# Kernel optimization log

Hardware: AMD Instinct MI355X
Metric: run time of the kernel (lower is better)

The kernel has to match this reference:

```python
import jax, jax.numpy as jnp
import numpy as np

N = 100000      # nodes
E = 1_600_000   # edges (avg degree 16)
IN, HID, OUT = 64, 64, 32


def setup_inputs() -> dict:
    key = jax.random.key(0)
    k1, k2, k3, k4, k5, k6 = jax.random.split(key, 6)
    x = jax.random.uniform(k1, (N, IN), dtype=jnp.float32)
    edge_index = jax.random.randint(k2, (2, E), 0, N, dtype=jnp.int32)
    # GCNConv weights (glorot-ish scale) and biases
    W1 = jax.random.normal(k3, (IN, HID), dtype=jnp.float32) * (1.0 / np.sqrt(IN))
    b1 = jnp.zeros((HID,), dtype=jnp.float32)
    W2 = jax.random.normal(k4, (HID, OUT), dtype=jnp.float32) * (1.0 / np.sqrt(HID))
    b2 = jnp.zeros((OUT,), dtype=jnp.float32)
    return {"x": x, "edge_index": edge_index, "W1": W1, "b1": b1, "W2": W2, "b2": b2}


def reference(x, edge_index, W1, b1, W2, b2):
    n = x.shape[0]
    # PyG GCNConv: add self-loops, symmetric deg^{-1/2} normalization
    loops = jnp.arange(n, dtype=edge_index.dtype)
    src = jnp.concatenate([edge_index[0], loops])  # message sources
    dst = jnp.concatenate([edge_index[1], loops])  # message targets
    ones = jnp.ones(src.shape[0], dtype=x.dtype)
    deg = jax.ops.segment_sum(ones, dst, num_segments=n)
    dinv = jnp.where(deg > 0, jax.lax.rsqrt(deg), 0.0)
    norm = dinv[src] * dinv[dst]  # [E+N]

    def gcn_conv(h, W, b):
        h = h @ W                          # [n, d_out]
        msg = h[src] * norm[:, None]       # gather + edge-normalize
        agg = jax.ops.segment_sum(msg, dst, num_segments=n)  # scatter-add
        return agg + b

    h = jax.nn.relu(gcn_conv(x, W1, b1))
    return gcn_conv(h, W2, b2)
```

## Files before the change

kernel.cpp:

```cpp
#include <hip/hip_runtime.h>
#include <hip/hip_fp16.h>


#define BSHIFT 8
#define BNODES 256
#define NB 256
#define CAP 5120

union H8 {
    uint4 u;
    __half2 h[4];
};

__device__ inline float2 u2f2(unsigned u) {
    union { unsigned x; __half2 h; } c;
    c.x = u;
    return __half22float2(c.h);
}
__device__ inline unsigned f2u(float a, float b) {
    union { unsigned x; __half2 h; } c;
    c.h = __floats2half2_rn(a, b);
    return c.x;
}

__global__ __launch_bounds__(256) void scatter_kernel(
    const int* __restrict__ src, const int* __restrict__ dst,
    int* __restrict__ cur, int* __restrict__ buf, int E) {
    __shared__ int h[512];
    __shared__ int curl[512];
    int t = threadIdx.x, b = blockIdx.x;
    for (int i = t; i < 512; i += 256) h[i] = 0;
    __syncthreads();
    int per = (E + NB - 1) / NB;
    int lo = b * per;
    int hi = min(lo + per, E);
    for (int i = lo + t; i < hi; i += 256) atomicAdd(&h[dst[i] >> BSHIFT], 1);
    __syncthreads();
    for (int i = t; i < 512; i += 256) {
        int c = h[i];
        curl[i] = c ? atomicAdd(&cur[i], c) : 0;
    }
    __syncthreads();
    for (int i = lo + t; i < hi; i += 256) {
        int d = dst[i];
        int bin = d >> BSHIFT;
        int loc = atomicAdd(&curl[bin], 1);
        if (loc < CAP)
            buf[(size_t)bin * CAP + loc] = (src[i] << BSHIFT) | (d & (BNODES - 1));
    }
}

__global__ __launch_bounds__(256) void bsort_kernel(
    const int* __restrict__ cur, int* __restrict__ buf,
    int2* __restrict__ off2, float* __restrict__ dinv, int N) {
    __shared__ int stage[CAP];
    __shared__ int h[BNODES];
    __shared__ int c2[BNODES];
    int t = threadIdx.x, b = blockIdx.x;
    int cnt = min(cur[b], CAP);
    int base = b * CAP;
    for (int i = t; i < cnt; i += 256) stage[i] = buf[base + i];
    h[t] = 0;
    __syncthreads();
    for (int i = t; i < cnt; i += 256)
        atomicAdd(&h[stage[i] & (BNODES - 1)], 1);
    __syncthreads();
    int deg = h[t];
#pragma unroll
    for (int d = 1; d < BNODES; d <<= 1) {
        int v = (t >= d) ? h[t - d] : 0;
        __syncthreads();
        h[t] += v;
        __syncthreads();
    }
    int excl = h[t] - deg;
    c2[t] = excl;
    int node = (b << BSHIFT) + t;
    if (node < N) {
        off2[node] = make_int2(base + excl, base + excl + deg);
        dinv[node] = rsqrtf((float)(deg + 1));
    }
    __syncthreads();
    for (int i = t; i < cnt; i += 256) {
        int p = stage[i];
        int pos = atomicAdd(&c2[p & (BNODES - 1)], 1);
        buf[base + pos] = p >> BSHIFT;
    }
}

__global__ __launch_bounds__(256) void gemm1_kernel(
    const float* __restrict__ x, const float* __restrict__ W1,
    const float* __restrict__ dinv, __half* __restrict__ hsh, int N) {
    __shared__ float4 Ws[64 * 16];
    int t = threadIdx.x;
    const float4* W4 = (const float4*)W1;
    for (int i = t; i < 1024; i += 256) Ws[i] = W4[i];
    __syncthreads();
    int c = t & 3;
    int rg = t >> 2;
    int r0 = blockIdx.x * 256 + rg * 4;
    if (r0 >= N) return;
    int nm1 = N - 1;
    float4 acc[4][4];
#pragma unroll
    for (int r = 0; r < 4; r++)
#pragma unroll
        for (int j = 0; j < 4; j++) acc[r][j] = make_float4(0.f, 0.f, 0.f, 0.f);
    const float4* x4 = (const float4*)x;
    for (int k4 = 0; k4 < 16; k4++) {
        float4 xv[4];
#pragma unroll
        for (int r = 0; r < 4; r++)
            xv[r] = x4[(size_t)min(r0 + r, nm1) * 16 + k4];
#pragma unroll
        for (int kk = 0; kk < 4; kk++) {
            const float4* wr = &Ws[(k4 * 4 + kk) * 16 + c * 4];
            float4 w0 = wr[0], w1 = wr[1], w2 = wr[2], w3 = wr[3];
#pragma unroll
            for (int r = 0; r < 4; r++) {
                float a = (kk == 0) ? xv[r].x : (kk == 1) ? xv[r].y
                          : (kk == 2) ? xv[r].z : xv[r].w;
                acc[r][0].x += a * w0.x; acc[r][0].y += a * w0.y;
                acc[r][0].z += a * w0.z; acc[r][0].w += a * w0.w;
                acc[r][1].x += a * w1.x; acc[r][1].y += a * w1.y;
                acc[r][1].z += a * w1.z; acc[r][1].w += a * w1.w;
                acc[r][2].x += a * w2.x; acc[r][2].y += a * w2.y;
                acc[r][2].z += a * w2.z; acc[r][2].w += a * w2.w;
                acc[r][3].x += a * w3.x; acc[r][3].y += a * w3.y;
                acc[r][3].z += a * w3.z; acc[r][3].w += a * w3.w;
            }
        }
    }
#pragma unroll
    for (int r = 0; r < 4; r++) {
        int row = r0 + r;
        if (row >= N) break;
        float di = dinv[row];
        uint4* ha = (uint4*)(hsh + (size_t)row * 64);
        H8 p0, p1;
        p0.h[0] = __floats2half2_rn(acc[r][0].x * di, acc[r][0].y * di);
        p0.h[1] = __floats2half2_rn(acc[r][0].z * di, acc[r][0].w * di);
        p0.h[2] = __floats2half2_rn(acc[r][1].x * di, acc[r][1].y * di);
        p0.h[3] = __floats2half2_rn(acc[r][1].z * di, acc[r][1].w * di);
        p1.h[0] = __floats2half2_rn(acc[r][2].x * di, acc[r][2].y * di);
        p1.h[1] = __floats2half2_rn(acc[r][2].z * di, acc[r][2].w * di);
        p1.h[2] = __floats2half2_rn(acc[r][3].x * di, acc[r][3].y * di);
        p1.h[3] = __floats2half2_rn(acc[r][3].z * di, acc[r][3].w * di);
        ha[c * 2 + 0] = p0.u;
        ha[c * 2 + 1] = p1.u;
    }
}

__global__ __launch_bounds__(256) void agg1gemm2_kernel(
    const uint4* __restrict__ hsh4, const int* __restrict__ ssrc,
    const int2* __restrict__ off2, const float* __restrict__ dinv,
    const float* __restrict__ b1, const float* __restrict__ W2,
    __half* __restrict__ gsh, int N) {
    __shared__ float4 Ws2[64 * 8];
    int t = threadIdx.x;
    const float4* W24 = (const float4*)W2;
    for (int i = t; i < 512; i += 256) Ws2[i] = W24[i];
    __syncthreads();
    int lane = t & 63;
    int wid = (blockIdx.x * 256 + t) >> 6;
    int node = wid * 8 + (lane >> 3);
    int fi = lane & 7;
    if (node >= N) return;
    int2 lh = off2[node];
    int lo = lh.x, hi = lh.y;
    float di = dinv[node];
    H8 sv;
    sv.u = hsh4[(size_t)node * 8 + fi];
    float2 a0 = __half22float2(sv.h[0]);
    float2 a1 = __half22float2(sv.h[1]);
    float2 a2 = __half22float2(sv.h[2]);
    float2 a3 = __half22float2(sv.h[3]);
    float2 c0 = make_float2(0.f, 0.f), c1 = make_float2(0.f, 0.f);
    float2 c2 = make_float2(0.f, 0.f), c3 = make_float2(0.f, 0.f);
    int hm1 = hi - 1;
    for (int e = lo; e < hi; e += 8) {
        int i1 = min(e + 1, hm1), i2 = min(e + 2, hm1), i3 = min(e + 3, hm1);
        int i4 = min(e + 4, hm1), i5 = min(e + 5, hm1), i6 = min(e + 6, hm1),
            i7 = min(e + 7, hm1);
        int s0 = __builtin_nontemporal_load(&ssrc[e]);
        int s1 = __builtin_nontemporal_load(&ssrc[i1]);
        int s2 = __builtin_nontemporal_load(&ssrc[i2]);
        int s3 = __builtin_nontemporal_load(&ssrc[i3]);
        int s4 = __builtin_nontemporal_load(&ssrc[i4]);
        int s5 = __builtin_nontemporal_load(&ssrc[i5]);
        int s6 = __builtin_nontemporal_load(&ssrc[i6]);
        int s7 = __builtin_nontemporal_load(&ssrc[i7]);
        H8 v0, v1, v2, v3, v4, v5, v6, v7;
        v0.u = hsh4[(size_t)s0 * 8 + fi];
        v1.u = hsh4[(size_t)s1 * 8 + fi];
        v2.u = hsh4[(size_t)s2 * 8 + fi];
        v3.u = hsh4[(size_t)s3 * 8 + fi];
        v4.u = hsh4[(size_t)s4 * 8 + fi];
        v5.u = hsh4[(size_t)s5 * 8 + fi];
        v6.u = hsh4[(size_t)s6 * 8 + fi];
        v7.u = hsh4[(size_t)s7 * 8 + fi];
        float m1 = (e + 1 < hi) ? 1.f : 0.f;
        float m2 = (e + 2 < hi) ? 1.f : 0.f;
        float m3 = (e + 3 < hi) ? 1.f : 0.f;
        float m4 = (e + 4 < hi) ? 1.f : 0.f;
        float m5 = (e + 5 < hi) ? 1.f : 0.f;
        float m6 = (e + 6 < hi) ? 1.f : 0.f;
        float m7 = (e + 7 < hi) ? 1.f : 0.f;
#pragma unroll
        for (int q = 0; q < 4; q++) {
            float2* aA = (q == 0) ? &a0 : (q == 1) ? &a1 : (q == 2) ? &a2 : &a3;
            float2* cA = (q == 0) ? &c0 : (q == 1) ? &c1 : (q == 2) ? &c2 : &c3;
            float2 f0 = __half22float2(v0.h[q]);
            float2 f1 = __half22float2(v1.h[q]);
            float2 f2 = __half22float2(v2.h[q]);
            float2 f3 = __half22float2(v3.h[q]);
            float2 f4 = __half22float2(v4.h[q]);
            float2 f5 = __half22float2(v5.h[q]);
            float2 f6 = __half22float2(v6.h[q]);
            float2 f7 = __half22float2(v7.h[q]);
            aA->x += f0.x + m1 * f1.x + m2 * f2.x + m3 * f3.x;
            aA->y += f0.y + m1 * f1.y + m2 * f2.y + m3 * f3.y;
            cA->x += m4 * f4.x + m5 * f5.x + m6 * f6.x + m7 * f7.x;
            cA->y += m4 * f4.y + m5 * f5.y + m6 * f6.y + m7 * f7.y;
        }
    }
    float4 bl = ((const float4*)b1)[fi * 2];
    float4 bh = ((const float4*)b1)[fi * 2 + 1];
    float r0 = fmaxf((a0.x + c0.x) * di + bl.x, 0.f);
    float r1 = fmaxf((a0.y + c0.y) * di + bl.y, 0.f);
    float r2 = fmaxf((a1.x + c1.x) * di + bl.z, 0.f);
    float r3 = fmaxf((a1.y + c1.y) * di + bl.w, 0.f);
    float r4 = fmaxf((a2.x + c2.x) * di + bh.x, 0.f);
    float r5 = fmaxf((a2.y + c2.y) * di + bh.y, 0.f);
    float r6 = fmaxf((a3.x + c3.x) * di + bh.z, 0.f);
    float r7 = fmaxf((a3.y + c3.y) * di + bh.w, 0.f);
    unsigned pk0 = f2u(r0, r1), pk1 = f2u(r2, r3);
    unsigned pk2 = f2u(r4, r5), pk3 = f2u(r6, r7);
    float4 acc2 = make_float4(0.f, 0.f, 0.f, 0.f);
#pragma unroll
    for (int s = 0; s < 8; s++) {
        int sl = (fi + s) & 7;
        unsigned u0 = __shfl(pk0, sl, 8);
        unsigned u1 = __shfl(pk1, sl, 8);
        unsigned u2 = __shfl(pk2, sl, 8);
        unsigned u3 = __shfl(pk3, sl, 8);
        float2 f0 = u2f2(u0), f1 = u2f2(u1), f2 = u2f2(u2), f3 = u2f2(u3);
        const float4* wr = &Ws2[sl * 64 + fi];
        float4 w;
        w = wr[0];
        acc2.x += f0.x * w.x; acc2.y += f0.x * w.y;
        acc2.z += f0.x * w.z; acc2.w += f0.x * w.w;
        w = wr[8];
        acc2.x += f0.y * w.x; acc2.y += f0.y * w.y;
        acc2.z += f0.y * w.z; acc2.w += f0.y * w.w;
        w = wr[16];
        acc2.x += f1.x * w.x; acc2.y += f1.x * w.y;
        acc2.z += f1.x * w.z; acc2.w += f1.x * w.w;
        w = wr[24];
        acc2.x += f1.y * w.x; acc2.y += f1.y * w.y;
        acc2.z += f1.y * w.z; acc2.w += f1.y * w.w;
        w = wr[32];
        acc2.x += f2.x * w.x; acc2.y += f2.x * w.y;
        acc2.z += f2.x * w.z; acc2.w += f2.x * w.w;
        w = wr[40];
        acc2.x += f2.y * w.x; acc2.y += f2.y * w.y;
        acc2.z += f2.y * w.z; acc2.w += f2.y * w.w;
        w = wr[48];
        acc2.x += f3.x * w.x; acc2.y += f3.x * w.y;
        acc2.z += f3.x * w.z; acc2.w += f3.x * w.w;
        w = wr[56];
        acc2.x += f3.y * w.x; acc2.y += f3.y * w.y;
        acc2.z += f3.y * w.z; acc2.w += f3.y * w.w;
    }
    uint2 pg;
    pg.x = f2u(acc2.x * di, acc2.y * di);
    pg.y = f2u(acc2.z * di, acc2.w * di);
    ((uint2*)gsh)[(size_t)node * 8 + fi] = pg;
}

__global__ __launch_bounds__(256) void agg2_kernel(
    const uint4* __restrict__ gsh4, const int* __restrict__ ssrc,
    const int2* __restrict__ off2, const float* __restrict__ dinv,
    const float* __restrict__ b2, float4* __restrict__ out4, int N) {
    int lane = threadIdx.x & 63;
    int wid = (blockIdx.x * 256 + threadIdx.x) >> 6;
    int node = wid * 16 + (lane >> 2);
    int fi = lane & 3;
    if (node >= N) return;
    int2 lh = off2[node];
    int lo = lh.x, hi = lh.y;
    float di = dinv[node];
    H8 sv;
    sv.u = gsh4[(size_t)node * 4 + fi];
    float2 a0 = __half22float2(sv.h[0]);
    float2 a1 = __half22float2(sv.h[1]);
    float2 a2 = __half22float2(sv.h[2]);
    float2 a3 = __half22float2(sv.h[3]);
    float2 c0 = make_float2(0.f, 0.f), c1 = make_float2(0.f, 0.f);
    float2 c2 = make_float2(0.f, 0.f), c3 = make_float2(0.f, 0.f);
    int hm1 = hi - 1;
    for (int e = lo; e < hi; e += 8) {
        int i1 = min(e + 1, hm1), i2 = min(e + 2, hm1), i3 = min(e + 3, hm1);
        int i4 = min(e + 4, hm1), i5 = min(e + 5, hm1), i6 = min(e + 6, hm1),
            i7 = min(e + 7, hm1);
        int s0 = __builtin_nontemporal_load(&ssrc[e]);
        int s1 = __builtin_nontemporal_load(&ssrc[i1]);
        int s2 = __builtin_nontemporal_load(&ssrc[i2]);
        int s3 = __builtin_nontemporal_load(&ssrc[i3]);
        int s4 = __builtin_nontemporal_load(&ssrc[i4]);
        int s5 = __builtin_nontemporal_load(&ssrc[i5]);
        int s6 = __builtin_nontemporal_load(&ssrc[i6]);
        int s7 = __builtin_nontemporal_load(&ssrc[i7]);
        H8 v0, v1, v2, v3, v4, v5, v6, v7;
        v0.u = gsh4[(size_t)s0 * 4 + fi];
        v1.u = gsh4[(size_t)s1 * 4 + fi];
        v2.u = gsh4[(size_t)s2 * 4 + fi];
        v3.u = gsh4[(size_t)s3 * 4 + fi];
        v4.u = gsh4[(size_t)s4 * 4 + fi];
        v5.u = gsh4[(size_t)s5 * 4 + fi];
        v6.u = gsh4[(size_t)s6 * 4 + fi];
        v7.u = gsh4[(size_t)s7 * 4 + fi];
        float m1 = (e + 1 < hi) ? 1.f : 0.f;
        float m2 = (e + 2 < hi) ? 1.f : 0.f;
        float m3 = (e + 3 < hi) ? 1.f : 0.f;
        float m4 = (e + 4 < hi) ? 1.f : 0.f;
        float m5 = (e + 5 < hi) ? 1.f : 0.f;
        float m6 = (e + 6 < hi) ? 1.f : 0.f;
        float m7 = (e + 7 < hi) ? 1.f : 0.f;
#pragma unroll
        for (int q = 0; q < 4; q++) {
            float2* aA = (q == 0) ? &a0 : (q == 1) ? &a1 : (q == 2) ? &a2 : &a3;
            float2* cA = (q == 0) ? &c0 : (q == 1) ? &c1 : (q == 2) ? &c2 : &c3;
            float2 f0 = __half22float2(v0.h[q]);
            float2 f1 = __half22float2(v1.h[q]);
            float2 f2 = __half22float2(v2.h[q]);
            float2 f3 = __half22float2(v3.h[q]);
            float2 f4 = __half22float2(v4.h[q]);
            float2 f5 = __half22float2(v5.h[q]);
            float2 f6 = __half22float2(v6.h[q]);
            float2 f7 = __half22float2(v7.h[q]);
            aA->x += f0.x + m1 * f1.x + m2 * f2.x + m3 * f3.x;
            aA->y += f0.y + m1 * f1.y + m2 * f2.y + m3 * f3.y;
            cA->x += m4 * f4.x + m5 * f5.x + m6 * f6.x + m7 * f7.x;
            cA->y += m4 * f4.y + m5 * f5.y + m6 * f6.y + m7 * f7.y;
        }
    }
    float4 bl = ((const float4*)b2)[fi * 2];
    float4 bh = ((const float4*)b2)[fi * 2 + 1];
    float4 r0, r1;
    r0.x = (a0.x + c0.x) * di + bl.x;
    r0.y = (a0.y + c0.y) * di + bl.y;
    r0.z = (a1.x + c1.x) * di + bl.z;
    r0.w = (a1.y + c1.y) * di + bl.w;
    r1.x = (a2.x + c2.x) * di + bh.x;
    r1.y = (a2.y + c2.y) * di + bh.y;
    r1.z = (a3.x + c3.x) * di + bh.z;
    r1.w = (a3.y + c3.y) * di + bh.w;
    out4[(size_t)node * 8 + fi * 2 + 0] = r0;
    out4[(size_t)node * 8 + fi * 2 + 1] = r1;
}

extern "C" void kernel_launch(void* const* d_in, const int* in_sizes, int n_in,
                              void* d_out, int out_size, void* d_ws,
                              size_t ws_size, hipStream_t stream) {
    const float* x  = (const float*)d_in[0];
    const int* ei   = (const int*)d_in[1];
    const float* W1 = (const float*)d_in[2];
    const float* b1 = (const float*)d_in[3];
    const float* W2 = (const float*)d_in[4];
    const float* b2 = (const float*)d_in[5];
    int N = in_sizes[0] / 64;
    int E = in_sizes[1] / 2;
    const int* src = ei;
    const int* dst = ei + E;
    int B = (N + BNODES - 1) >> BSHIFT;

    char* ws = (char*)d_ws;
    size_t o = 0;
    auto align16 = [&o]() { o = (o + 15) & ~(size_t)15; };
    int* cur    = (int*)(ws + o); o += 512 * 4; align16();
    int* buf    = (int*)(ws + o); o += (size_t)B * CAP * 4; align16();
    int2* off2  = (int2*)(ws + o); o += (size_t)N * 8; align16();
    float* dinv = (float*)(ws + o); o += (size_t)N * 4; align16();
    __half* hsh = (__half*)(ws + o); o += (size_t)N * 64 * 2; align16();
    __half* gsh = (__half*)(ws + o); o += (size_t)N * 32 * 2; align16();
    float* outp = (float*)d_out;

    hipMemsetAsync(cur, 0, 512 * 4, stream);
    scatter_kernel<<<NB, 256, 0, stream>>>(src, dst, cur, buf, E);
    bsort_kernel<<<B, 256, 0, stream>>>(cur, buf, off2, dinv, N);
    gemm1_kernel<<<(N + 255) / 256, 256, 0, stream>>>(x, W1, dinv, hsh, N);
    agg1gemm2_kernel<<<(N + 31) / 32, 256, 0, stream>>>(
        (const uint4*)hsh, buf, off2, dinv, b1, W2, gsh, N);
    agg2_kernel<<<(N + 63) / 64, 256, 0, stream>>>(
        (const uint4*)gsh, buf, off2, dinv, b2, (float4*)outp, N);
}
```

Before: 207.4 us.

## Bucket nodes by degree class to balance warp work in aggregation kernels

The sort kernel now groups nodes into eight degree classes (in steps of 8 edges) and writes a per-class node order list with global class counts. Both aggregation kernels map thread groups to nodes through this order, so nodes sharing a wavefront have similar edge counts and loop trip counts. The aim is less divergence and idle lanes in the edge loops. In exchange it adds an indirection lookup per node, extra atomics and writes in bsort, and loses the locality of consecutive node IDs for the per-node loads and output stores.

```diff
diff --git a/kernel.cpp b/kernel.cpp
--- a/kernel.cpp
+++ b/kernel.cpp
@@ -21,6 +21,18 @@
     union { unsigned x; __half2 h; } c;
     c.h = __floats2half2_rn(a, b);
     return c.x;
+}
+
+__device__ inline int rank_to_node(int g, const int* __restrict__ clscnt,
+                                   const int* __restrict__ order, int N) {
+    int pre = 0, node = -1;
+#pragma unroll
+    for (int c = 0; c < 8; c++) {
+        int cc = clscnt[c];
+        if (node < 0 && g < pre + cc) node = order[c * N + (g - pre)];
+        pre += cc;
+    }
+    return node;
 }
 
 __global__ __launch_bounds__(256) void scatter_kernel(
@@ -52,20 +64,29 @@
 
 __global__ __launch_bounds__(256) void bsort_kernel(
     const int* __restrict__ cur, int* __restrict__ buf,
-    int2* __restrict__ off2, float* __restrict__ dinv, int N) {
+    int2* __restrict__ off2, float* __restrict__ dinv,
+    int* __restrict__ order, int* __restrict__ clscnt, int N) {
     __shared__ int stage[CAP];
     __shared__ int h[BNODES];
     __shared__ int c2[BNODES];
+    __shared__ int ch[8];
+    __shared__ int cbase[8];
     int t = threadIdx.x, b = blockIdx.x;
     int cnt = min(cur[b], CAP);
     int base = b * CAP;
     for (int i = t; i < cnt; i += 256) stage[i] = buf[base + i];
     h[t] = 0;
+    if (t < 8) ch[t] = 0;
     __syncthreads();
     for (int i = t; i < cnt; i += 256)
         atomicAdd(&h[stage[i] & (BNODES - 1)], 1);
     __syncthreads();
     int deg = h[t];
+    int node = (b << BSHIFT) + t;
+    bool valid = node < N;
+    int cls = min((deg + 7) >> 3, 7);
+    int loc = 0;
+    if (valid) loc = atomicAdd(&ch[cls], 1);
 #pragma unroll
     for (int d = 1; d < BNODES; d <<= 1) {
         int v = (t >= d) ? h[t - d] : 0;
@@ -75,12 +96,13 @@
     }
     int excl = h[t] - deg;
     c2[t] = excl;
-    int node = (b << BSHIFT) + t;
-    if (node < N) {
+    if (t < 8) cbase[t] = ch[t] ? atomicAdd(&clscnt[t], ch[t]) : 0;
+    if (valid) {
         off2[node] = make_int2(base + excl, base + excl + deg);
         dinv[node] = rsqrtf((float)(deg + 1));
     }
     __syncthreads();
+    if (valid) order[cls * N + cbase[cls] + loc] = node;
     for (int i = t; i < cnt; i += 256) {
         int p = stage[i];
         int pos = atomicAdd(&c2[p & (BNODES - 1)], 1);
@@ -154,6 +176,7 @@
 __global__ __launch_bounds__(256) void agg1gemm2_kernel(
     const uint4* __restrict__ hsh4, const int* __restrict__ ssrc,
     const int2* __restrict__ off2, const float* __restrict__ dinv,
+    const int* __restrict__ order, const int* __restrict__ clscnt,
     const float* __restrict__ b1, const float* __restrict__ W2,
     __half* __restrict__ gsh, int N) {
     __shared__ float4 Ws2[64 * 8];
@@ -163,9 +186,10 @@
     __syncthreads();
     int lane = t & 63;
     int wid = (blockIdx.x * 256 + t) >> 6;
-    int node = wid * 8 + (lane >> 3);
+    int g = wid * 8 + (lane >> 3);
     int fi = lane & 7;
-    if (node >= N) return;
+    if (g >= N) return;
+    int node = rank_to_node(g, clscnt, order, N);
     int2 lh = off2[node];
     int lo = lh.x, hi = lh.y;
     float di = dinv[node];
@@ -281,12 +305,14 @@
 __global__ __launch_bounds__(256) void agg2_kernel(
     const uint4* __restrict__ gsh4, const int* __restrict__ ssrc,
     const int2* __restrict__ off2, const float* __restrict__ dinv,
+    const int* __restrict__ order, const int* __restrict__ clscnt,
     const float* __restrict__ b2, float4* __restrict__ out4, int N) {
     int lane = threadIdx.x & 63;
     int wid = (blockIdx.x * 256 + threadIdx.x) >> 6;
-    int node = wid * 16 + (lane >> 2);
+    int g = wid * 16 + (lane >> 2);
     int fi = lane & 3;
-    if (node >= N) return;
+    if (g >= N) return;
+    int node = rank_to_node(g, clscnt, order, N);
     int2 lh = off2[node];
     int lo = lh.x, hi = lh.y;
     float di = dinv[node];
@@ -378,20 +404,24 @@
     char* ws = (char*)d_ws;
     size_t o = 0;
     auto align16 = [&o]() { o = (o + 15) & ~(size_t)15; };
-    int* cur    = (int*)(ws + o); o += 512 * 4; align16();
+    int* cur    = (int*)(ws + o); o += 520 * 4; align16();
+    int* clscnt = cur + 512;
     int* buf    = (int*)(ws + o); o += (size_t)B * CAP * 4; align16();
     int2* off2  = (int2*)(ws + o); o += (size_t)N * 8; align16();
     float* dinv = (float*)(ws + o); o += (size_t)N * 4; align16();
+    int* order  = (int*)(ws + o); o += (size_t)N * 8 * 4; align16();
     __half* hsh = (__half*)(ws + o); o += (size_t)N * 64 * 2; align16();
     __half* gsh = (__half*)(ws + o); o += (size_t)N * 32 * 2; align16();
     float* outp = (float*)d_out;
 
-    hipMemsetAsync(cur, 0, 512 * 4, stream);
+    hipMemsetAsync(cur, 0, 520 * 4, stream);
     scatter_kernel<<<NB, 256, 0, stream>>>(src, dst, cur, buf, E);
-    bsort_kernel<<<B, 256, 0, stream>>>(cur, buf, off2, dinv, N);
+    bsort_kernel<<<B, 256, 0, stream>>>(cur, buf, off2, dinv, order, clscnt,
+                                        N);
     gemm1_kernel<<<(N + 255) / 256, 256, 0, stream>>>(x, W1, dinv, hsh, N);
     agg1gemm2_kernel<<<(N + 31) / 32, 256, 0, stream>>>(
-        (const uint4*)hsh, buf, off2, dinv, b1, W2, gsh, N);
+        (const uint4*)hsh, buf, off2, dinv, order, clscnt, b1, W2, gsh, N);
     agg2_kernel<<<(N + 63) / 64, 256, 0, stream>>>(
-        (const uint4*)gsh, buf, off2, dinv, b2, (float4*)outp, N);
-}
+        (const uint4*)gsh, buf, off2, dinv, order, clscnt, b2, (float4*)outp,
+        N);
+}
```

Result: slower. 239.3 us (+15.4%).

## Compute degrees in scatter via global atomics and co-launch bucket sort with gemm1

Applied to the files above, without the earlier changes.

The scatter kernel now counts per-node in-degree with global atomics, so degrees are known before the bucket sort. That lets the bucket sort and the first GEMM, which no longer depends on sort output, run as disjoint block ranges of a single launch. dinv is recomputed on the fly from deg with rsqrtf instead of being stored. This removes one kernel launch and serialization point. In exchange it adds 1.6M global atomics in scatter and a larger memset.

```diff
diff --git a/kernel.cpp b/kernel.cpp
--- a/kernel.cpp
+++ b/kernel.cpp
@@ -25,7 +25,8 @@
 
 __global__ __launch_bounds__(256) void scatter_kernel(
     const int* __restrict__ src, const int* __restrict__ dst,
-    int* __restrict__ cur, int* __restrict__ buf, int E) {
+    int* __restrict__ cur, int* __restrict__ deg, int* __restrict__ buf,
+    int E) {
     __shared__ int h[512];
     __shared__ int curl[512];
     int t = threadIdx.x, b = blockIdx.x;
@@ -47,113 +48,111 @@
         int loc = atomicAdd(&curl[bin], 1);
         if (loc < CAP)
             buf[(size_t)bin * CAP + loc] = (src[i] << BSHIFT) | (d & (BNODES - 1));
-    }
-}
-
-__global__ __launch_bounds__(256) void bsort_kernel(
+        atomicAdd(&deg[d], 1);
+    }
+}
+
+__global__ __launch_bounds__(256) void sortgemm_kernel(
     const int* __restrict__ cur, int* __restrict__ buf,
-    int2* __restrict__ off2, float* __restrict__ dinv, int N) {
-    __shared__ int stage[CAP];
-    __shared__ int h[BNODES];
-    __shared__ int c2[BNODES];
-    int t = threadIdx.x, b = blockIdx.x;
-    int cnt = min(cur[b], CAP);
-    int base = b * CAP;
-    for (int i = t; i < cnt; i += 256) stage[i] = buf[base + i];
-    h[t] = 0;
-    __syncthreads();
-    for (int i = t; i < cnt; i += 256)
-        atomicAdd(&h[stage[i] & (BNODES - 1)], 1);
-    __syncthreads();
-    int deg = h[t];
-#pragma unroll
-    for (int d = 1; d < BNODES; d <<= 1) {
-        int v = (t >= d) ? h[t - d] : 0;
+    const int* __restrict__ deg, int2* __restrict__ off2,
+    const float* __restrict__ x, const float* __restrict__ W1,
+    __half* __restrict__ hsh, int N, int B) {
+    __shared__ int smem[CAP + 512];
+    int t = threadIdx.x;
+    if ((int)blockIdx.x < B) {
+        int b = blockIdx.x;
+        int* stage = smem;
+        int* c2 = smem + CAP;
+        int* sc = smem + CAP + 256;
+        int cnt = min(cur[b], CAP);
+        int base = b * CAP;
+        for (int i = t; i < cnt; i += 256) stage[i] = buf[base + i];
+        int node = (b << BSHIFT) + t;
+        int dg = (node < N) ? deg[node] : 0;
+        sc[t] = dg;
         __syncthreads();
-        h[t] += v;
+#pragma unroll
+        for (int d = 1; d < BNODES; d <<= 1) {
+            int v = (t >= d) ? sc[t - d] : 0;
+            __syncthreads();
+            sc[t] += v;
+            __syncthreads();
+        }
+        int excl = sc[t] - dg;
+        c2[t] = excl;
+        if (node < N)
+            off2[node] = make_int2(base + excl, base + excl + dg);
         __syncthreads();
-    }
-    int excl = h[t] - deg;
-    c2[t] = excl;
-    int node = (b << BSHIFT) + t;
-    if (node < N) {
-        off2[node] = make_int2(base + excl, base + excl + deg);
-        dinv[node] = rsqrtf((float)(deg + 1));
-    }
-    __syncthreads();
-    for (int i = t; i < cnt; i += 256) {
-        int p = stage[i];
-        int pos = atomicAdd(&c2[p & (BNODES - 1)], 1);
-        buf[base + pos] = p >> BSHIFT;
-    }
-}
-
-__global__ __launch_bounds__(256) void gemm1_kernel(
-    const float* __restrict__ x, const float* __restrict__ W1,
-    const float* __restrict__ dinv, __half* __restrict__ hsh, int N) {
-    __shared__ float4 Ws[64 * 16];
-    int t = threadIdx.x;
-    const float4* W4 = (const float4*)W1;
-    for (int i = t; i < 1024; i += 256) Ws[i] = W4[i];
-    __syncthreads();
-    int c = t & 3;
-    int rg = t >> 2;
-    int r0 = blockIdx.x * 256 + rg * 4;
-    if (r0 >= N) return;
-    int nm1 = N - 1;
-    float4 acc[4][4];
-#pragma unroll
-    for (int r = 0; r < 4; r++)
-#pragma unroll
-        for (int j = 0; j < 4; j++) acc[r][j] = make_float4(0.f, 0.f, 0.f, 0.f);
-    const float4* x4 = (const float4*)x;
-    for (int k4 = 0; k4 < 16; k4++) {
-        float4 xv[4];
+        for (int i = t; i < cnt; i += 256) {
+            int p = stage[i];
+            int pos = atomicAdd(&c2[p & (BNODES - 1)], 1);
+            buf[base + pos] = p >> BSHIFT;
+        }
+    } else {
+        float4* Ws = (float4*)smem;
+        const float4* W4 = (const float4*)W1;
+        for (int i = t; i < 1024; i += 256) Ws[i] = W4[i];
+        __syncthreads();
+        int c = t & 3;
+        int rg = t >> 2;
+        int r0 = ((int)blockIdx.x - B) * 256 + rg * 4;
+        if (r0 >= N) return;
+        int nm1 = N - 1;
+        float4 acc[4][4];
 #pragma unroll
         for (int r = 0; r < 4; r++)
-            xv[r] = x4[(size_t)min(r0 + r, nm1) * 16 + k4];
-#pragma unroll
-        for (int kk = 0; kk < 4; kk++) {
-            const float4* wr = &Ws[(k4 * 4 + kk) * 16 + c * 4];
-            float4 w0 = wr[0], w1 = wr[1], w2 = wr[2], w3 = wr[3];
-#pragma unroll
-            for (int r = 0; r < 4; r++) {
-                float a = (kk == 0) ? xv[r].x : (kk == 1) ? xv[r].y
-                          : (kk == 2) ? xv[r].z : xv[r].w;
-                acc[r][0].x += a * w0.x; acc[r][0].y += a * w0.y;
-                acc[r][0].z += a * w0.z; acc[r][0].w += a * w0.w;
-                acc[r][1].x += a * w1.x; acc[r][1].y += a * w1.y;
-                acc[r][1].z += a * w1.z; acc[r][1].w += a * w1.w;
-                acc[r][2].x += a * w2.x; acc[r][2].y += a * w2.y;
-                acc[r][2].z += a * w2.z; acc[r][2].w += a * w2.w;
-                acc[r][3].x += a * w3.x; acc[r][3].y += a * w3.y;
-                acc[r][3].z += a * w3.z; acc[r][3].w += a * w3.w;
+#pragma unroll
+            for (int j = 0; j < 4; j++)
+                acc[r][j] = make_float4(0.f, 0.f, 0.f, 0.f);
+        const float4* x4 = (const float4*)x;
+        for (int k4 = 0; k4 < 16; k4++) {
+            float4 xv[4];
+#pragma unroll
+            for (int r = 0; r < 4; r++)
+                xv[r] = x4[(size_t)min(r0 + r, nm1) * 16 + k4];
+#pragma unroll
+            for (int kk = 0; kk < 4; kk++) {
+                const float4* wr = &Ws[(k4 * 4 + kk) * 16 + c * 4];
+                float4 w0 = wr[0], w1 = wr[1], w2 = wr[2], w3 = wr[3];
+#pragma unroll
+                for (int r = 0; r < 4; r++) {
+                    float a = (kk == 0) ? xv[r].x : (kk == 1) ? xv[r].y
+                              : (kk == 2) ? xv[r].z : xv[r].w;
+                    acc[r][0].x += a * w0.x; acc[r][0].y += a * w0.y;
+                    acc[r][0].z += a * w0.z; acc[r][0].w += a * w0.w;
+                    acc[r][1].x += a * w1.x; acc[r][1].y += a * w1.y;
+                    acc[r][1].z += a * w1.z; acc[r][1].w += a * w1.w;
+                    acc[r][2].x += a * w2.x; acc[r][2].y += a * w2.y;
+                    acc[r][2].z += a * w2.z; acc[r][2].w += a * w2.w;
+                    acc[r][3].x += a * w3.x; acc[r][3].y += a * w3.y;
+                    acc[r][3].z += a * w3.z; acc[r][3].w += a * w3.w;
+                }
             }
         }
-    }
-#pragma unroll
-    for (int r = 0; r < 4; r++) {
-        int row = r0 + r;
-        if (row >= N) break;
-        float di = dinv[row];
-        uint4* ha = (uint4*)(hsh + (size_t)row * 64);
-        H8 p0, p1;
-        p0.h[0] = __floats2half2_rn(acc[r][0].x * di, acc[r][0].y * di);
-        p0.h[1] = __floats2half2_rn(acc[r][0].z * di, acc[r][0].w * di);
-        p0.h[2] = __floats2half2_rn(acc[r][1].x * di, acc[r][1].y * di);
-        p0.h[3] = __floats2half2_rn(acc[r][1].z * di, acc[r][1].w * di);
-        p1.h[0] = __floats2half2_rn(acc[r][2].x * di, acc[r][2].y * di);
-        p1.h[1] = __floats2half2_rn(acc[r][2].z * di, acc[r][2].w * di);
-        p1.h[2] = __floats2half2_rn(acc[r][3].x * di, acc[r][3].y * di);
-        p1.h[3] = __floats2half2_rn(acc[r][3].z * di, acc[r][3].w * di);
-        ha[c * 2 + 0] = p0.u;
-        ha[c * 2 + 1] = p1.u;
+#pragma unroll
+        for (int r = 0; r < 4; r++) {
+            int row = r0 + r;
+            if (row >= N) break;
+            float di = rsqrtf((float)(deg[row] + 1));
+            uint4* ha = (uint4*)(hsh + (size_t)row * 64);
+            H8 p0, p1;
+            p0.h[0] = __floats2half2_rn(acc[r][0].x * di, acc[r][0].y * di);
+            p0.h[1] = __floats2half2_rn(acc[r][0].z * di, acc[r][0].w * di);
+            p0.h[2] = __floats2half2_rn(acc[r][1].x * di, acc[r][1].y * di);
+            p0.h[3] = __floats2half2_rn(acc[r][1].z * di, acc[r][1].w * di);
+            p1.h[0] = __floats2half2_rn(acc[r][2].x * di, acc[r][2].y * di);
+            p1.h[1] = __floats2half2_rn(acc[r][2].z * di, acc[r][2].w * di);
+            p1.h[2] = __floats2half2_rn(acc[r][3].x * di, acc[r][3].y * di);
+            p1.h[3] = __floats2half2_rn(acc[r][3].z * di, acc[r][3].w * di);
+            ha[c * 2 + 0] = p0.u;
+            ha[c * 2 + 1] = p1.u;
+        }
     }
 }
 
 __global__ __launch_bounds__(256) void agg1gemm2_kernel(
     const uint4* __restrict__ hsh4, const int* __restrict__ ssrc,
-    const int2* __restrict__ off2, const float* __restrict__ dinv,
+    const int2* __restrict__ off2, const int* __restrict__ deg,
     const float* __restrict__ b1, const float* __restrict__ W2,
     __half* __restrict__ gsh, int N) {
     __shared__ float4 Ws2[64 * 8];
@@ -168,7 +167,7 @@
     if (node >= N) return;
     int2 lh = off2[node];
     int lo = lh.x, hi = lh.y;
-    float di = dinv[node];
+    float di = rsqrtf((float)(deg[node] + 1));
     H8 sv;
     sv.u = hsh4[(size_t)node * 8 + fi];
     float2 a0 = __half22float2(sv.h[0]);
@@ -280,7 +279,7 @@
 
 __global__ __launch_bounds__(256) void agg2_kernel(
     const uint4* __restrict__ gsh4, const int* __restrict__ ssrc,
-    const int2* __restrict__ off2, const float* __restrict__ dinv,
+    const int2* __restrict__ off2, const int* __restrict__ deg,
     const float* __restrict__ b2, float4* __restrict__ out4, int N) {
     int lane = threadIdx.x & 63;
     int wid = (blockIdx.x * 256 + threadIdx.x) >> 6;
@@ -289,7 +288,7 @@
     if (node >= N) return;
     int2 lh = off2[node];
     int lo = lh.x, hi = lh.y;
-    float di = dinv[node];
+    float di = rsqrtf((float)(deg[node] + 1));
     H8 sv;
     sv.u = gsh4[(size_t)node * 4 + fi];
     float2 a0 = __half22float2(sv.h[0]);
@@ -374,24 +373,25 @@
     const int* src = ei;
     const int* dst = ei + E;
     int B = (N + BNODES - 1) >> BSHIFT;
+    int G = (N + 255) / 256;
 
     char* ws = (char*)d_ws;
     size_t o = 0;
     auto align16 = [&o]() { o = (o + 15) & ~(size_t)15; };
-    int* cur    = (int*)(ws + o); o += 512 * 4; align16();
+    int* cur    = (int*)(ws + o); o += 512 * 4;
+    int* deg    = (int*)(ws + o); o += (size_t)N * 4; align16();
     int* buf    = (int*)(ws + o); o += (size_t)B * CAP * 4; align16();
     int2* off2  = (int2*)(ws + o); o += (size_t)N * 8; align16();
-    float* dinv = (float*)(ws + o); o += (size_t)N * 4; align16();
     __half* hsh = (__half*)(ws + o); o += (size_t)N * 64 * 2; align16();
     __half* gsh = (__half*)(ws + o); o += (size_t)N * 32 * 2; align16();
     float* outp = (float*)d_out;
 
-    hipMemsetAsync(cur, 0, 512 * 4, stream);
-    scatter_kernel<<<NB, 256, 0, stream>>>(src, dst, cur, buf, E);
-    bsort_kernel<<<B, 256, 0, stream>>>(cur, buf, off2, dinv, N);
-    gemm1_kernel<<<(N + 255) / 256, 256, 0, stream>>>(x, W1, dinv, hsh, N);
+    hipMemsetAsync(cur, 0, (512 + (size_t)N) * 4, stream);
+    scatter_kernel<<<NB, 256, 0, stream>>>(src, dst, cur, deg, buf, E);
+    sortgemm_kernel<<<B + G, 256, 0, stream>>>(cur, buf, deg, off2, x, W1,
+                                               hsh, N, B);
     agg1gemm2_kernel<<<(N + 31) / 32, 256, 0, stream>>>(
-        (const uint4*)hsh, buf, off2, dinv, b1, W2, gsh, N);
+        (const uint4*)hsh, buf, off2, deg, b1, W2, gsh, N);
     agg2_kernel<<<(N + 63) / 64, 256, 0, stream>>>(
-        (const uint4*)gsh, buf, off2, dinv, b2, (float4*)outp, N);
-}
+        (const uint4*)gsh, buf, off2, deg, b2, (float4*)outp, N);
+}
```

Measured after the change: 254.2 us. 1.23x slower.

## Fuse GCN pipeline into one cooperative persistent kernel with grid syncs

Applied to the files above, without the earlier changes.

Replaces the memset plus five separate kernel launches with a single cooperative kernel. Each former stage runs as a phase over grid-strided work, and phases are separated by grid.sync(). The aim is to remove launch gaps and per-kernel ramp-up and tail costs. In exchange, the grid is limited to the blocks that can be co-resident, each grid sync adds barrier latency, and the 22KB of shared memory may limit occupancy in the gather phases. The old multi-kernel path is kept as a fallback if the cooperative launch fails.

```diff
diff --git a/kernel.cpp b/kernel.cpp
--- a/kernel.cpp
+++ b/kernel.cpp
@@ -1,5 +1,8 @@
 #include <hip/hip_runtime.h>
 #include <hip/hip_fp16.h>
+#include <hip/hip_cooperative_groups.h>
+
+namespace cg = cooperative_groups;
 
 
 #define BSHIFT 8
@@ -21,6 +24,362 @@
     union { unsigned x; __half2 h; } c;
     c.h = __floats2half2_rn(a, b);
     return c.x;
+}
+
+__global__ __launch_bounds__(256, 4) void gcn_mega(
+    const int* __restrict__ src, const int* __restrict__ dst,
+    int* __restrict__ cur, int* __restrict__ buf, int2* __restrict__ off2,
+    float* __restrict__ dinv, const float* __restrict__ x,
+    const float* __restrict__ W1, __half* __restrict__ hsh,
+    const float* __restrict__ b1, const float* __restrict__ W2,
+    __half* __restrict__ gsh, const float* __restrict__ b2,
+    float4* __restrict__ out4, int N, int E, int B) {
+    cg::grid_group grid = cg::this_grid();
+    __shared__ int smem[CAP + 512];
+    int t = threadIdx.x;
+    int b = blockIdx.x;
+    int nb = gridDim.x;
+
+    int* h = smem;
+    int* curl = smem + 512;
+    for (int i = t; i < 512; i += 256) h[i] = 0;
+    if (b == 0)
+        for (int i = t; i < 512; i += 256) cur[i] = 0;
+    int per = (E + nb - 1) / nb;
+    int lo = b * per;
+    int hi = min(lo + per, E);
+    __syncthreads();
+    for (int i = lo + t; i < hi; i += 256) atomicAdd(&h[dst[i] >> BSHIFT], 1);
+    grid.sync();
+    for (int i = t; i < 512; i += 256) {
+        int c = h[i];
+        curl[i] = c ? atomicAdd(&cur[i], c) : 0;
+    }
+    __syncthreads();
+    for (int i = lo + t; i < hi; i += 256) {
+        int d = dst[i];
+        int bin = d >> BSHIFT;
+        int loc = atomicAdd(&curl[bin], 1);
+        if (loc < CAP)
+            buf[(size_t)bin * CAP + loc] =
+                (src[i] << BSHIFT) | (d & (BNODES - 1));
+    }
+    grid.sync();
+
+    for (int bb = b; bb < B; bb += nb) {
+        int* stage = smem;
+        int* hh = smem + CAP;
+        int* c2 = smem + CAP + 256;
+        int cnt = min(cur[bb], CAP);
+        int base = bb * CAP;
+        for (int i = t; i < cnt; i += 256) stage[i] = buf[base + i];
+        hh[t] = 0;
+        __syncthreads();
+        for (int i = t; i < cnt; i += 256)
+            atomicAdd(&hh[stage[i] & (BNODES - 1)], 1);
+        __syncthreads();
+        int deg = hh[t];
+#pragma unroll
+        for (int d = 1; d < BNODES; d <<= 1) {
+            int v = (t >= d) ? hh[t - d] : 0;
+            __syncthreads();
+            hh[t] += v;
+            __syncthreads();
+        }
+        int excl = hh[t] - deg;
+        c2[t] = excl;
+        int node = (bb << BSHIFT) + t;
+        if (node < N) {
+            off2[node] = make_int2(base + excl, base + excl + deg);
+            dinv[node] = rsqrtf((float)(deg + 1));
+        }
+        __syncthreads();
+        for (int i = t; i < cnt; i += 256) {
+            int p = stage[i];
+            int pos = atomicAdd(&c2[p & (BNODES - 1)], 1);
+            buf[base + pos] = p >> BSHIFT;
+        }
+        __syncthreads();
+    }
+    grid.sync();
+
+    {
+        float4* Ws = (float4*)smem;
+        const float4* W4 = (const float4*)W1;
+        for (int i = t; i < 1024; i += 256) Ws[i] = W4[i];
+        __syncthreads();
+        int c = t & 3;
+        int rg = t >> 2;
+        int U = (N + 127) >> 7;
+        int nm1 = N - 1;
+        const float4* x4 = (const float4*)x;
+        for (int u = b; u < U; u += nb) {
+            int r0 = u * 128 + rg * 2;
+            if (r0 >= N) continue;
+            float4 acc[2][4];
+#pragma unroll
+            for (int r = 0; r < 2; r++)
+#pragma unroll
+                for (int j = 0; j < 4; j++)
+                    acc[r][j] = make_float4(0.f, 0.f, 0.f, 0.f);
+            for (int k4 = 0; k4 < 16; k4++) {
+                float4 xv0 = x4[(size_t)min(r0, nm1) * 16 + k4];
+                float4 xv1 = x4[(size_t)min(r0 + 1, nm1) * 16 + k4];
+#pragma unroll
+                for (int kk = 0; kk < 4; kk++) {
+                    const float4* wr = &Ws[(k4 * 4 + kk) * 16 + c * 4];
+                    float4 w0 = wr[0], w1 = wr[1], w2 = wr[2], w3 = wr[3];
+                    float a0 = (kk == 0) ? xv0.x : (kk == 1) ? xv0.y
+                               : (kk == 2) ? xv0.z : xv0.w;
+                    float a1 = (kk == 0) ? xv1.x : (kk == 1) ? xv1.y
+                               : (kk == 2) ? xv1.z : xv1.w;
+                    acc[0][0].x += a0 * w0.x; acc[0][0].y += a0 * w0.y;
+                    acc[0][0].z += a0 * w0.z; acc[0][0].w += a0 * w0.w;
+                    acc[0][1].x += a0 * w1.x; acc[0][1].y += a0 * w1.y;
+                    acc[0][1].z += a0 * w1.z; acc[0][1].w += a0 * w1.w;
+                    acc[0][2].x += a0 * w2.x; acc[0][2].y += a0 * w2.y;
+                    acc[0][2].z += a0 * w2.z; acc[0][2].w += a0 * w2.w;
+                    acc[0][3].x += a0 * w3.x; acc[0][3].y += a0 * w3.y;
+                    acc[0][3].z += a0 * w3.z; acc[0][3].w += a0 * w3.w;
+                    acc[1][0].x += a1 * w0.x; acc[1][0].y += a1 * w0.y;
+                    acc[1][0].z += a1 * w0.z; acc[1][0].w += a1 * w0.w;
+                    acc[1][1].x += a1 * w1.x; acc[1][1].y += a1 * w1.y;
+                    acc[1][1].z += a1 * w1.z; acc[1][1].w += a1 * w1.w;
+                    acc[1][2].x += a1 * w2.x; acc[1][2].y += a1 * w2.y;
+                    acc[1][2].z += a1 * w2.z; acc[1][2].w += a1 * w2.w;
+                    acc[1][3].x += a1 * w3.x; acc[1][3].y += a1 * w3.y;
+                    acc[1][3].z += a1 * w3.z; acc[1][3].w += a1 * w3.w;
+                }
+            }
+#pragma unroll
+            for (int r = 0; r < 2; r++) {
+                int row = r0 + r;
+                if (row >= N) break;
+                float di = dinv[row];
+                uint4* ha = (uint4*)(hsh + (size_t)row * 64);
+                H8 p0, p1;
+                p0.h[0] = __floats2half2_rn(acc[r][0].x * di, acc[r][0].y * di);
+                p0.h[1] = __floats2half2_rn(acc[r][0].z * di, acc[r][0].w * di);
+                p0.h[2] = __floats2half2_rn(acc[r][1].x * di, acc[r][1].y * di);
+                p0.h[3] = __floats2half2_rn(acc[r][1].z * di, acc[r][1].w * di);
+                p1.h[0] = __floats2half2_rn(acc[r][2].x * di, acc[r][2].y * di);
+                p1.h[1] = __floats2half2_rn(acc[r][2].z * di, acc[r][2].w * di);
+                p1.h[2] = __floats2half2_rn(acc[r][3].x * di, acc[r][3].y * di);
+                p1.h[3] = __floats2half2_rn(acc[r][3].z * di, acc[r][3].w * di);
+                ha[c * 2 + 0] = p0.u;
+                ha[c * 2 + 1] = p1.u;
+            }
+        }
+    }
+    grid.sync();
+
+    {
+        const uint4* hsh4 = (const uint4*)hsh;
+        const int* ssrc = buf;
+        float4* Ws2 = (float4*)smem;
+        const float4* W24 = (const float4*)W2;
+        __syncthreads();
+        for (int i = t; i < 512; i += 256) Ws2[i] = W24[i];
+        __syncthreads();
+        int lane = t & 63;
+        int fi = lane & 7;
+        int U = (N + 31) >> 5;
+        for (int u = b; u < U; u += nb) {
+            int wid = u * 4 + (t >> 6);
+            int node = wid * 8 + (lane >> 3);
+            if (node >= N) continue;
+            int2 lh = off2[node];
+            int elo = lh.x, ehi = lh.y;
+            float di = dinv[node];
+            H8 sv;
+            sv.u = hsh4[(size_t)node * 8 + fi];
+            float2 a0 = __half22float2(sv.h[0]);
+            float2 a1 = __half22float2(sv.h[1]);
+            float2 a2 = __half22float2(sv.h[2]);
+            float2 a3 = __half22float2(sv.h[3]);
+            float2 c0 = make_float2(0.f, 0.f), c1 = make_float2(0.f, 0.f);
+            float2 c2 = make_float2(0.f, 0.f), c3 = make_float2(0.f, 0.f);
+            int hm1 = ehi - 1;
+            for (int e = elo; e < ehi; e += 8) {
+                int i1 = min(e + 1, hm1), i2 = min(e + 2, hm1),
+                    i3 = min(e + 3, hm1);
+                int i4 = min(e + 4, hm1), i5 = min(e + 5, hm1),
+                    i6 = min(e + 6, hm1), i7 = min(e + 7, hm1);
+                int s0 = ssrc[e], s1 = ssrc[i1], s2 = ssrc[i2], s3 = ssrc[i3];
+                int s4 = ssrc[i4], s5 = ssrc[i5], s6 = ssrc[i6], s7 = ssrc[i7];
+                H8 v0, v1, v2, v3, v4, v5, v6, v7;
+                v0.u = hsh4[(size_t)s0 * 8 + fi];
+                v1.u = hsh4[(size_t)s1 * 8 + fi];
+                v2.u = hsh4[(size_t)s2 * 8 + fi];
+                v3.u = hsh4[(size_t)s3 * 8 + fi];
+                v4.u = hsh4[(size_t)s4 * 8 + fi];
+                v5.u = hsh4[(size_t)s5 * 8 + fi];
+                v6.u = hsh4[(size_t)s6 * 8 + fi];
+                v7.u = hsh4[(size_t)s7 * 8 + fi];
+                float m1 = (e + 1 < ehi) ? 1.f : 0.f;
+                float m2 = (e + 2 < ehi) ? 1.f : 0.f;
+                float m3 = (e + 3 < ehi) ? 1.f : 0.f;
+                float m4 = (e + 4 < ehi) ? 1.f : 0.f;
+                float m5 = (e + 5 < ehi) ? 1.f : 0.f;
+                float m6 = (e + 6 < ehi) ? 1.f : 0.f;
+                float m7 = (e + 7 < ehi) ? 1.f : 0.f;
+#pragma unroll
+                for (int q = 0; q < 4; q++) {
+                    float2* aA = (q == 0) ? &a0 : (q == 1) ? &a1
+                                          : (q == 2) ? &a2 : &a3;
+                    float2* cA = (q == 0) ? &c0 : (q == 1) ? &c1
+                                          : (q == 2) ? &c2 : &c3;
+                    float2 f0 = __half22float2(v0.h[q]);
+                    float2 f1 = __half22float2(v1.h[q]);
+                    float2 f2 = __half22float2(v2.h[q]);
+                    float2 f3 = __half22float2(v3.h[q]);
+                    float2 f4 = __half22float2(v4.h[q]);
+                    float2 f5 = __half22float2(v5.h[q]);
+                    float2 f6 = __half22float2(v6.h[q]);
+                    float2 f7 = __half22float2(v7.h[q]);
+                    aA->x += f0.x + m1 * f1.x + m2 * f2.x + m3 * f3.x;
+                    aA->y += f0.y + m1 * f1.y + m2 * f2.y + m3 * f3.y;
+                    cA->x += m4 * f4.x + m5 * f5.x + m6 * f6.x + m7 * f7.x;
+                    cA->y += m4 * f4.y + m5 * f5.y + m6 * f6.y + m7 * f7.y;
+                }
+            }
+            float4 bl = ((const float4*)b1)[fi * 2];
+            float4 bh = ((const float4*)b1)[fi * 2 + 1];
+            float r0 = fmaxf((a0.x + c0.x) * di + bl.x, 0.f);
+            float r1 = fmaxf((a0.y + c0.y) * di + bl.y, 0.f);
+            float r2 = fmaxf((a1.x + c1.x) * di + bl.z, 0.f);
+            float r3 = fmaxf((a1.y + c1.y) * di + bl.w, 0.f);
+            float r4 = fmaxf((a2.x + c2.x) * di + bh.x, 0.f);
+            float r5 = fmaxf((a2.y + c2.y) * di + bh.y, 0.f);
+            float r6 = fmaxf((a3.x + c3.x) * di + bh.z, 0.f);
+            float r7 = fmaxf((a3.y + c3.y) * di + bh.w, 0.f);
+            unsigned pk0 = f2u(r0, r1), pk1 = f2u(r2, r3);
+            unsigned pk2 = f2u(r4, r5), pk3 = f2u(r6, r7);
+            float4 acc2 = make_float4(0.f, 0.f, 0.f, 0.f);
+#pragma unroll
+            for (int s = 0; s < 8; s++) {
+                int sl = (fi + s) & 7;
+                unsigned u0 = __shfl(pk0, sl, 8);
+                unsigned u1 = __shfl(pk1, sl, 8);
+                unsigned u2 = __shfl(pk2, sl, 8);
+                unsigned u3 = __shfl(pk3, sl, 8);
+                float2 f0 = u2f2(u0), f1 = u2f2(u1), f2 = u2f2(u2),
+                       f3 = u2f2(u3);
+                const float4* wr = &Ws2[sl * 64 + fi];
+                float4 w;
+                w = wr[0];
+                acc2.x += f0.x * w.x; acc2.y += f0.x * w.y;
+                acc2.z += f0.x * w.z; acc2.w += f0.x * w.w;
+                w = wr[8];
+                acc2.x += f0.y * w.x; acc2.y += f0.y * w.y;
+                acc2.z += f0.y * w.z; acc2.w += f0.y * w.w;
+                w = wr[16];
+                acc2.x += f1.x * w.x; acc2.y += f1.x * w.y;
+                acc2.z += f1.x * w.z; acc2.w += f1.x * w.w;
+                w = wr[24];
+                acc2.x += f1.y * w.x; acc2.y += f1.y * w.y;
+                acc2.z += f1.y * w.z; acc2.w += f1.y * w.w;
+                w = wr[32];
+                acc2.x += f2.x * w.x; acc2.y += f2.x * w.y;
+                acc2.z += f2.x * w.z; acc2.w += f2.x * w.w;
+                w = wr[40];
+                acc2.x += f2.y * w.x; acc2.y += f2.y * w.y;
+                acc2.z += f2.y * w.z; acc2.w += f2.y * w.w;
+                w = wr[48];
+                acc2.x += f3.x * w.x; acc2.y += f3.x * w.y;
+                acc2.z += f3.x * w.z; acc2.w += f3.x * w.w;
+                w = wr[56];
+                acc2.x += f3.y * w.x; acc2.y += f3.y * w.y;
+                acc2.z += f3.y * w.z; acc2.w += f3.y * w.w;
+            }
+            uint2 pg;
+            pg.x = f2u(acc2.x * di, acc2.y * di);
+            pg.y = f2u(acc2.z * di, acc2.w * di);
+            ((uint2*)gsh)[(size_t)node * 8 + fi] = pg;
+        }
+    }
+    grid.sync();
+
+    {
+        const uint4* gsh4 = (const uint4*)gsh;
+        const int* ssrc = buf;
+        int lane = t & 63;
+        int fi = lane & 3;
+        int U = (N + 63) >> 6;
+        for (int u = b; u < U; u += nb) {
+            int wid = u * 4 + (t >> 6);
+            int node = wid * 16 + (lane >> 2);
+            if (node >= N) continue;
+            int2 lh = off2[node];
+            int elo = lh.x, ehi = lh.y;
+            float di = dinv[node];
+            H8 sv;
+            sv.u = gsh4[(size_t)node * 4 + fi];
+            float2 a0 = __half22float2(sv.h[0]);
+            float2 a1 = __half22float2(sv.h[1]);
+            float2 a2 = __half22float2(sv.h[2]);
+            float2 a3 = __half22float2(sv.h[3]);
+            float2 c0 = make_float2(0.f, 0.f), c1 = make_float2(0.f, 0.f);
+            float2 c2 = make_float2(0.f, 0.f), c3 = make_float2(0.f, 0.f);
+            int hm1 = ehi - 1;
+            for (int e = elo; e < ehi; e += 8) {
+                int i1 = min(e + 1, hm1), i2 = min(e + 2, hm1),
+                    i3 = min(e + 3, hm1);
+                int i4 = min(e + 4, hm1), i5 = min(e + 5, hm1),
+                    i6 = min(e + 6, hm1), i7 = min(e + 7, hm1);
+                int s0 = ssrc[e], s1 = ssrc[i1], s2 = ssrc[i2], s3 = ssrc[i3];
+                int s4 = ssrc[i4], s5 = ssrc[i5], s6 = ssrc[i6], s7 = ssrc[i7];
+                H8 v0, v1, v2, v3, v4, v5, v6, v7;
+                v0.u = gsh4[(size_t)s0 * 4 + fi];
+                v1.u = gsh4[(size_t)s1 * 4 + fi];
+                v2.u = gsh4[(size_t)s2 * 4 + fi];
+                v3.u = gsh4[(size_t)s3 * 4 + fi];
+                v4.u = gsh4[(size_t)s4 * 4 + fi];
+                v5.u = gsh4[(size_t)s5 * 4 + fi];
+                v6.u = gsh4[(size_t)s6 * 4 + fi];
+                v7.u = gsh4[(size_t)s7 * 4 + fi];
+                float m1 = (e + 1 < ehi) ? 1.f : 0.f;
+                float m2 = (e + 2 < ehi) ? 1.f : 0.f;
+                float m3 = (e + 3 < ehi) ? 1.f : 0.f;
+                float m4 = (e + 4 < ehi) ? 1.f : 0.f;
+                float m5 = (e + 5 < ehi) ? 1.f : 0.f;
+                float m6 = (e + 6 < ehi) ? 1.f : 0.f;
+                float m7 = (e + 7 < ehi) ? 1.f : 0.f;
+#pragma unroll
+                for (int q = 0; q < 4; q++) {
+                    float2* aA = (q == 0) ? &a0 : (q == 1) ? &a1
+                                          : (q == 2) ? &a2 : &a3;
+                    float2* cA = (q == 0) ? &c0 : (q == 1) ? &c1
+                                          : (q == 2) ? &c2 : &c3;
+                    float2 f0 = __half22float2(v0.h[q]);
+                    float2 f1 = __half22float2(v1.h[q]);
+                    float2 f2 = __half22float2(v2.h[q]);
+                    float2 f3 = __half22float2(v3.h[q]);
+                    float2 f4 = __half22float2(v4.h[q]);
+                    float2 f5 = __half22float2(v5.h[q]);
+                    float2 f6 = __half22float2(v6.h[q]);
+                    float2 f7 = __half22float2(v7.h[q]);
+                    aA->x += f0.x + m1 * f1.x + m2 * f2.x + m3 * f3.x;
+                    aA->y += f0.y + m1 * f1.y + m2 * f2.y + m3 * f3.y;
+                    cA->x += m4 * f4.x + m5 * f5.x + m6 * f6.x + m7 * f7.x;
+                    cA->y += m4 * f4.y + m5 * f5.y + m6 * f6.y + m7 * f7.y;
+                }
+            }
+            float4 bl = ((const float4*)b2)[fi * 2];
+            float4 bh = ((const float4*)b2)[fi * 2 + 1];
+            float4 r0, r1;
+            r0.x = (a0.x + c0.x) * di + bl.x;
+            r0.y = (a0.y + c0.y) * di + bl.y;
+            r0.z = (a1.x + c1.x) * di + bl.z;
+            r0.w = (a1.y + c1.y) * di + bl.w;
+            r1.x = (a2.x + c2.x) * di + bh.x;
+            r1.y = (a2.y + c2.y) * di + bh.y;
+            r1.z = (a3.x + c3.x) * di + bh.z;
+            r1.w = (a3.y + c3.y) * di + bh.w;
+            out4[(size_t)node * 8 + fi * 2 + 0] = r0;
+            out4[(size_t)node * 8 + fi * 2 + 1] = r1;
+        }
+    }
 }
 
 __global__ __launch_bounds__(256) void scatter_kernel(
@@ -384,14 +743,43 @@
     float* dinv = (float*)(ws + o); o += (size_t)N * 4; align16();
     __half* hsh = (__half*)(ws + o); o += (size_t)N * 64 * 2; align16();
     __half* gsh = (__half*)(ws + o); o += (size_t)N * 32 * 2; align16();
-    float* outp = (float*)d_out;
-
-    hipMemsetAsync(cur, 0, 512 * 4, stream);
-    scatter_kernel<<<NB, 256, 0, stream>>>(src, dst, cur, buf, E);
-    bsort_kernel<<<B, 256, 0, stream>>>(cur, buf, off2, dinv, N);
-    gemm1_kernel<<<(N + 255) / 256, 256, 0, stream>>>(x, W1, dinv, hsh, N);
-    agg1gemm2_kernel<<<(N + 31) / 32, 256, 0, stream>>>(
-        (const uint4*)hsh, buf, off2, dinv, b1, W2, gsh, N);
-    agg2_kernel<<<(N + 63) / 64, 256, 0, stream>>>(
-        (const uint4*)gsh, buf, off2, dinv, b2, (float4*)outp, N);
-}
+    float4* outp = (float4*)d_out;
+
+    static int s_grid = -2;
+    if (s_grid == -2) {
+        int nbpc = 0;
+        hipError_t e1 = hipOccupancyMaxActiveBlocksPerMultiprocessor(
+            &nbpc, (const void*)gcn_mega, 256, 0);
+        hipDeviceProp_t prop;
+        hipError_t e2 = hipGetDeviceProperties(&prop, 0);
+        if (e1 == hipSuccess && e2 == hipSuccess && nbpc > 0)
+            s_grid = nbpc * prop.multiProcessorCount;
+        else
+            s_grid = 0;
+    }
+    bool coop_ok = false;
+    if (s_grid > 0) {
+        void* args[] = {(void*)&src,  (void*)&dst, (void*)&cur, (void*)&buf,
+                        (void*)&off2, (void*)&dinv, (void*)&x,  (void*)&W1,
+                        (void*)&hsh,  (void*)&b1,  (void*)&W2,  (void*)&gsh,
+                        (void*)&b2,   (void*)&outp, (void*)&N,  (void*)&E,
+                        (void*)&B};
+        hipError_t e = hipLaunchCooperativeKernel(
+            (const void*)gcn_mega, dim3(s_grid), dim3(256), args, 0, stream);
+        if (e == hipSuccess) {
+            coop_ok = true;
+        } else {
+            s_grid = 0;
+        }
+    }
+    if (!coop_ok) {
+        hipMemsetAsync(cur, 0, 512 * 4, stream);
+        scatter_kernel<<<NB, 256, 0, stream>>>(src, dst, cur, buf, E);
+        bsort_kernel<<<B, 256, 0, stream>>>(cur, buf, off2, dinv, N);
+        gemm1_kernel<<<(N + 255) / 256, 256, 0, stream>>>(x, W1, dinv, hsh, N);
+        agg1gemm2_kernel<<<(N + 31) / 32, 256, 0, stream>>>(
+            (const uint4*)hsh, buf, off2, dinv, b1, W2, gsh, N);
+        agg2_kernel<<<(N + 63) / 64, 256, 0, stream>>>(
+            (const uint4*)gsh, buf, off2, dinv, b2, outp, N);
+    }
+}
```

Measured after the change: 510.6 us. +146.2%, slower.
